# Performance work log

Hardware: AMD Instinct MI355X
Metric: run time of the kernel (lower is better)

## Reference

```python
import jax, jax.numpy as jnp
import numpy as np

# Model dims (see init_kwargs)
E = 512        # embedding_dim
H = 1536       # hidden_dim
SIZE = 4       # state_space.size (state types per layer)
S = 32         # choices per state type (uniform state size)
L = 12         # num_layers of child network
T = SIZE * L   # total controller steps = 48
V = SIZE * S   # num_embeddings = 128


def setup_inputs() -> dict:
    key = jax.random.key(0)
    ks = jax.random.split(key, 12)
    sc = 0.05
    f32 = jnp.float32
    return {
        "input_id": 0,
        "emb":   (jax.random.normal(ks[0], (V, E)) * sc).astype(f32),
        "W_ih1": (jax.random.normal(ks[1], (4 * H, E)) * sc).astype(f32),
        "W_hh1": (jax.random.normal(ks[2], (4 * H, H)) * sc).astype(f32),
        "b_ih1": (jax.random.normal(ks[3], (4 * H,)) * sc).astype(f32),
        "b_hh1": (jax.random.normal(ks[4], (4 * H,)) * sc).astype(f32),
        "W_ih2": (jax.random.normal(ks[5], (4 * H, H)) * sc).astype(f32),
        "W_hh2": (jax.random.normal(ks[6], (4 * H, H)) * sc).astype(f32),
        "b_ih2": (jax.random.normal(ks[7], (4 * H,)) * sc).astype(f32),
        "b_hh2": (jax.random.normal(ks[8], (4 * H,)) * sc).astype(f32),
        "W_out": (jax.random.normal(ks[9], (T, S, H)) * sc).astype(f32),
        "b_out": (jax.random.normal(ks[10], (T, S)) * sc).astype(f32),
    }


def _lstm_cell(x, h, c, Wih, Whh, bih, bhh):
    # torch.nn.LSTMCell: gates ordered (i, f, g, o)
    g = x @ Wih.T + bih + h @ Whh.T + bhh
    gi, gf, gg, go = jnp.split(g, 4)
    c_new = jax.nn.sigmoid(gf) * c + jax.nn.sigmoid(gi) * jnp.tanh(gg)
    h_new = jax.nn.sigmoid(go) * jnp.tanh(c_new)
    return h_new, c_new


def reference(input_id, emb, W_ih1, W_hh1, b_ih1, b_hh1,
              W_ih2, W_hh2, b_ih2, b_hh2, W_out, b_out):
    x0 = emb[input_id]                      # [E]
    z = jnp.zeros((H,), emb.dtype)

    def step(carry, inp):
        i, Wo, bo = inp                     # Wo: [S,H], bo: [S]
        x, h1, c1, h2, c2 = carry
        h1, c1 = _lstm_cell(x, h1, c1, W_ih1, W_hh1, b_ih1, b_hh1)
        h2, c2 = _lstm_cell(h1, h2, c2, W_ih2, W_hh2, b_ih2, b_hh2)
        logp = jax.nn.log_softmax(Wo @ h2 + bo)   # [S]
        pred = jnp.argmax(logp)
        emb_id = (i % SIZE) * S + pred            # state-space embedding id
        x_next = emb[emb_id]
        return (x_next, h1, c1, h2, c2), logp

    _, scores = jax.lax.scan(step, (x0, z, z, z, z),
                             (jnp.arange(T), W_out, b_out))
    return scores  # [T, S] log-probabilities
```

## Files before the change

### kernel.cpp

```cpp
#include <hip/hip_runtime.h>
#include <math.h>

#define H 1536
#define E 512
#define T 48
#define S 32
#define V 128
#define NB 256
#define BT 512
#define JPB 6
#define ROWS 24
#define RPW 3
#define CHK 24
#define WHH2_B   (64 * 145 * 16)
#define HBUF_B   (64 * 7 * 16)
#define DYN_LDS  (WHH2_B + HBUF_B)

#define LOG_W   4096
#define H2_W    20480
#define CAND_W  24576
#define XW1_W   122880

__device__ __forceinline__ float sigf(float x) { return 1.0f / (1.0f + expf(-x)); }
__device__ __forceinline__ float wred(float acc) {
#pragma unroll
    for (int off = 32; off; off >>= 1) acc += __shfl_down(acc, off);
    return acc;
}

#define GLD(p)    __hip_atomic_load((p), __ATOMIC_RELAXED, __HIP_MEMORY_SCOPE_AGENT)
#define GST(p, v) __hip_atomic_store((p), (v), __ATOMIC_RELAXED, __HIP_MEMORY_SCOPE_AGENT)

__device__ __forceinline__ void gbar(unsigned* ctr, unsigned& gen) {
    __syncthreads();
    gen++;
    if (threadIdx.x == 0)
        __hip_atomic_fetch_add(&ctr[(blockIdx.x & 7) * 16], 1u,
                               __ATOMIC_RELAXED, __HIP_MEMORY_SCOPE_AGENT);
    if (threadIdx.x < 8) {
        const unsigned tgt = gen * 32u;
        while (GLD(&ctr[threadIdx.x * 16]) < tgt)
            __builtin_amdgcn_s_sleep(1);
    }
    __syncthreads();
}

__global__ __launch_bounds__(BT, 1) void nas_persist(
    const int* __restrict__ input_id, const float* __restrict__ emb,
    const float* __restrict__ Wih1, const float* __restrict__ Whh1,
    const float* __restrict__ bih1, const float* __restrict__ bhh1,
    const float* __restrict__ Wih2, const float* __restrict__ Whh2,
    const float* __restrict__ bih2, const float* __restrict__ bhh2,
    const float* __restrict__ Wout, const float* __restrict__ bout,
    float* __restrict__ out, float* __restrict__ ws)
{
    const int b = blockIdx.x, tid = threadIdx.x;
    const int wave = tid >> 6, lane = tid & 63;

    unsigned* ctr = (unsigned*)ws;
    float* logitp = ws + LOG_W;
    float* h2gp[2]  = { ws + H2_W,   ws + H2_W + H };
    float* candp[2] = { ws + CAND_W, ws + CAND_W + S * H };
    float* xw1g = ws + XW1_W + (size_t)b * (V * ROWS);

    extern __shared__ char dyn_lds[];
    float4* whh2s = (float4*)dyn_lds;
    float*  hbuf  = (float*)(dyn_lds + WHH2_B);

    __shared__ float gacc1[ROWS], g2f[ROWS], bsum2[ROWS], zlog[S], h2f[JPB];
    __shared__ float c1s[JPB], c2s[JPB], c1cand[S * JPB];
    __shared__ int   xid_s, pred_s;

    unsigned gen = 0;

    if (tid < JPB) { c2s[tid] = 0.f; GST(h2gp[0] + b * JPB + tid, 0.f); }
    if (tid < ROWS) {
        int r = (tid / JPB) * H + b * JPB + (tid % JPB);
        bsum2[tid] = bih2[r] + bhh2[r];
    }
    if (tid == 0) xid_s = *input_id;

    {
        const int k0 = wave * RPW;
        float4 wiA[RPW], wiB[RPW];
        float  bs[RPW];
#pragma unroll
        for (int i = 0; i < RPW; ++i) {
            int k = k0 + i;
            int r = (k / JPB) * H + b * JPB + (k % JPB);
            const float4* w = (const float4*)(Wih1 + (size_t)r * E);
            wiA[i] = w[lane]; wiB[i] = w[lane + 64];
            bs[i]  = bih1[r] + bhh1[r];
        }
        float4* stage = (float4*)dyn_lds;
        for (int ch = 0; ch < 8; ++ch) {
            const float4* src = (const float4*)(emb + (size_t)ch * 16 * E);
            for (int m = tid; m < 2048; m += BT) stage[m] = src[m];
            __syncthreads();
            for (int vv = 0; vv < 16; ++vv) {
                float4 ea = stage[vv * 128 + lane];
                float4 eb = stage[vv * 128 + 64 + lane];
#pragma unroll
                for (int i = 0; i < RPW; ++i) {
                    float a = wiA[i].x * ea.x + wiA[i].y * ea.y + wiA[i].z * ea.z + wiA[i].w * ea.w
                            + wiB[i].x * eb.x + wiB[i].y * eb.y + wiB[i].z * eb.z + wiB[i].w * eb.w;
                    a = wred(a);
                    if (lane == 0) xw1g[(ch * 16 + vv) * ROWS + (k0 + i)] = a + bs[i];
                }
            }
            __syncthreads();
        }
    }

    for (int k = 0; k < ROWS; ++k) {
        int r = (k / JPB) * H + b * JPB + (k % JPB);
        const float4* src = (const float4*)(Whh2 + (size_t)r * H);
        if (tid < 384) {
            int l = tid / 6, j = tid % 6;
            whh2s[l * 145 + k * 6 + j] = src[tid];
        }
    }
    __syncthreads();

    float w1[RPW][CHK], w2[RPW][CHK];
#pragma unroll
    for (int i = 0; i < RPW; ++i) {
        int k = wave * RPW + i;
        int r = (k / JPB) * H + b * JPB + (k % JPB);
        const float4* p1 = (const float4*)(Whh1 + (size_t)r * H) + lane * 6;
        const float4* p2 = (const float4*)(Wih2 + (size_t)r * H) + lane * 6;
#pragma unroll
        for (int j = 0; j < 6; ++j) {
            float4 v1 = p1[j], v2 = p2[j];
            w1[i][4 * j + 0] = v1.x; w1[i][4 * j + 1] = v1.y;
            w1[i][4 * j + 2] = v1.z; w1[i][4 * j + 3] = v1.w;
            w2[i][4 * j + 0] = v2.x; w2[i][4 * j + 1] = v2.y;
            w2[i][4 * j + 2] = v2.z; w2[i][4 * j + 3] = v2.w;
        }
    }
    __syncthreads();

    if (tid < JPB) {
        const float* xr = xw1g + (size_t)xid_s * ROWS;
        float gi = xr[tid], gg = xr[2 * JPB + tid], go = xr[3 * JPB + tid];
        float cn = sigf(gi) * tanhf(gg);
        c1s[tid] = cn;
        GST(candp[0] + b * JPB + tid, sigf(go) * tanhf(cn));
    }
    gbar(ctr, gen);

    const int m0 = (tid / CHK) * 28 + (tid % CHK);
    const int m1 = ((tid + 512) / CHK) * 28 + ((tid + 512) % CHK);
    const int m2 = ((tid + 1024) / CHK) * 28 + ((tid + 1024) % CHK);

    for (int k = 0; k <= T; ++k) {
        float pv[16];
        const float* lp = logitp + (size_t)(k & 1) * (S * NB)
                          + (tid >> 4) * NB + (tid & 15) * 16;
        if (k > 0) {
#pragma unroll
            for (int i = 0; i < 16; ++i) pv[i] = GLD(lp + i);
        }
        const float* h2src = h2gp[k & 1];
        float u0 = GLD(h2src + tid);
        float u1 = GLD(h2src + tid + 512);
        float u2 = GLD(h2src + tid + 1024);
        float wcol[JPB];
        if (k < T && wave == 0 && lane < S) {
            const float* wp = Wout + ((size_t)k * S + lane) * H + b * JPB;
#pragma unroll
            for (int j = 0; j < JPB; ++j) wcol[j] = wp[j];
        }

        if (k > 0) {
            float acc = 0.f;
#pragma unroll
            for (int i = 0; i < 16; ++i) acc += pv[i];
#pragma unroll
            for (int off = 8; off; off >>= 1) acc += __shfl_down(acc, off, 16);
            if ((tid & 15) == 0)
                zlog[tid >> 4] = acc + bout[(size_t)(k - 1) * S + (tid >> 4)];
        }
        __syncthreads();
        if (k > 0) {
            if (wave == 0) {
                float z = (lane < S) ? zlog[lane] : -1e30f;
                float v = z; int idx = (lane < S) ? lane : 9999;
#pragma unroll
                for (int off = 32; off; off >>= 1) {
                    float ov = __shfl_xor(v, off); int oi = __shfl_xor(idx, off);
                    if (ov > v || (ov == v && oi < idx)) { v = ov; idx = oi; }
                }
                float e = (lane < S) ? expf(z - v) : 0.f;
#pragma unroll
                for (int off = 32; off; off >>= 1) e += __shfl_xor(e, off);
                if (lane == 0) pred_s = idx;
                if (b == 0 && lane < S) out[(size_t)(k - 1) * S + lane] = z - v - logf(e);
            }
            __syncthreads();
        }
        if (k == T) return;
        const int psel = (k > 0) ? pred_s : 0;
        if (k > 0 && tid < JPB) c1s[tid] = c1cand[psel * JPB + tid];

        const float* h1src = candp[k & 1] + (size_t)psel * H;
        float t0 = GLD(h1src + tid);
        float t1 = GLD(h1src + tid + 512);
        float t2 = GLD(h1src + tid + 1024);

        hbuf[m0] = u0; hbuf[m1] = u1; hbuf[m2] = u2;
        __syncthreads();
        float h2c[CHK];
        {
            const float4* hp = (const float4*)hbuf + lane * 7;
#pragma unroll
            for (int j = 0; j < 6; ++j) {
                float4 v = hp[j];
                h2c[4 * j + 0] = v.x; h2c[4 * j + 1] = v.y;
                h2c[4 * j + 2] = v.z; h2c[4 * j + 3] = v.w;
            }
        }
        float ahv[RPW];
#pragma unroll
        for (int i = 0; i < RPW; ++i) {
            int kk = wave * RPW + i;
            const float4* wp = whh2s + lane * 145 + kk * 6;
            float ah = 0.f;
#pragma unroll
            for (int j = 0; j < 6; ++j) {
                float4 v = wp[j];
                ah += v.x * h2c[4 * j + 0] + v.y * h2c[4 * j + 1]
                    + v.z * h2c[4 * j + 2] + v.w * h2c[4 * j + 3];
            }
            ahv[i] = wred(ah);
        }
        __syncthreads();
        hbuf[m0] = t0; hbuf[m1] = t1; hbuf[m2] = t2;
        __syncthreads();
        float h1c[CHK];
        {
            const float4* hp = (const float4*)hbuf + lane * 7;
#pragma unroll
            for (int j = 0; j < 6; ++j) {
                float4 v = hp[j];
                h1c[4 * j + 0] = v.x; h1c[4 * j + 1] = v.y;
                h1c[4 * j + 2] = v.z; h1c[4 * j + 3] = v.w;
            }
        }
        float a1[RPW], a2[RPW];
#pragma unroll
        for (int i = 0; i < RPW; ++i) { a1[i] = 0.f; a2[i] = 0.f; }
#pragma unroll
        for (int kk = 0; kk < CHK; ++kk) {
            float h = h1c[kk];
#pragma unroll
            for (int i = 0; i < RPW; ++i) {
                a1[i] += w1[i][kk] * h;
                a2[i] += w2[i][kk] * h;
            }
        }
#pragma unroll
        for (int i = 0; i < RPW; ++i) {
            int kk = wave * RPW + i;
            float s1 = wred(a1[i]);
            float s2 = wred(a2[i]);
            if (lane == 0) {
                gacc1[kk] = s1;
                g2f[kk]   = s2 + ahv[i] + bsum2[kk];
            }
        }
        __syncthreads();

        if (tid < JPB) {
            float gi = g2f[tid],           gf = g2f[JPB + tid];
            float gg = g2f[2 * JPB + tid], go = g2f[3 * JPB + tid];
            float cn = sigf(gf) * c2s[tid] + sigf(gi) * tanhf(gg);
            c2s[tid] = cn;
            float hn = sigf(go) * tanhf(cn);
            h2f[tid] = hn;
            GST(h2gp[(k + 1) & 1] + b * JPB + tid, hn);
        }
        if (tid < S * JPB) {
            int p = tid / JPB, j = tid % JPB;
            const float* xr = xw1g + (size_t)((k & 3) * S + p) * ROWS;
            float gi = gacc1[j]           + xr[j];
            float gf = gacc1[JPB + j]     + xr[JPB + j];
            float gg = gacc1[2 * JPB + j] + xr[2 * JPB + j];
            float go = gacc1[3 * JPB + j] + xr[3 * JPB + j];
            float cn = sigf(gf) * c1s[j] + sigf(gi) * tanhf(gg);
            c1cand[tid] = cn;
            GST(candp[(k + 1) & 1] + (size_t)p * H + b * JPB + j,
                sigf(go) * tanhf(cn));
        }
        __syncthreads();
        if (wave == 0 && lane < S) {
            float p = 0.f;
#pragma unroll
            for (int j = 0; j < JPB; ++j) p += wcol[j] * h2f[j];
            GST(logitp + (size_t)((k + 1) & 1) * (S * NB) + lane * NB + b, p);
        }
        gbar(ctr, gen);
    }
}

extern "C" void kernel_launch(void* const* d_in, const int* in_sizes, int n_in,
                              void* d_out, int out_size, void* d_ws, size_t ws_size,
                              hipStream_t stream) {
    const int*   input_id = (const int*)d_in[0];
    const float* emb  = (const float*)d_in[1];
    const float* Wih1 = (const float*)d_in[2];
    const float* Whh1 = (const float*)d_in[3];
    const float* bih1 = (const float*)d_in[4];
    const float* bhh1 = (const float*)d_in[5];
    const float* Wih2 = (const float*)d_in[6];
    const float* Whh2 = (const float*)d_in[7];
    const float* bih2 = (const float*)d_in[8];
    const float* bhh2 = (const float*)d_in[9];
    const float* Wout = (const float*)d_in[10];
    const float* bout = (const float*)d_in[11];
    float* out = (float*)d_out;
    float* ws  = (float*)d_ws;

    hipMemsetAsync(d_ws, 0, 512, stream);

    void* args[] = { (void*)&input_id, (void*)&emb,
                     (void*)&Wih1, (void*)&Whh1, (void*)&bih1, (void*)&bhh1,
                     (void*)&Wih2, (void*)&Whh2, (void*)&bih2, (void*)&bhh2,
                     (void*)&Wout, (void*)&bout, (void*)&out, (void*)&ws };
    hipLaunchCooperativeKernel((void*)nas_persist, dim3(NB), dim3(BT), args,
                               DYN_LDS, stream);
}
```

Measured before the change: 1.207 ms.

## Replace atomic grid barrier with generation-tagged logit partials as dataflow flags

```diff
diff --git a/kernel.cpp b/kernel.cpp
--- a/kernel.cpp
+++ b/kernel.cpp
@@ -16,10 +16,11 @@
 #define HBUF_B   (64 * 7 * 16)
 #define DYN_LDS  (WHH2_B + HBUF_B)
 
-#define LOG_W   4096
-#define H2_W    20480
-#define CAND_W  24576
-#define XW1_W   122880
+typedef unsigned long long u64;
+
+#define H2_W    32768
+#define CAND_W  36864
+#define XW1_W   135168
 
 __device__ __forceinline__ float sigf(float x) { return 1.0f / (1.0f + expf(-x)); }
 __device__ __forceinline__ float wred(float acc) {
@@ -28,24 +29,18 @@
     return acc;
 }
 
-#define GLD(p)    __hip_atomic_load((p), __ATOMIC_RELAXED, __HIP_MEMORY_SCOPE_AGENT)
-#define GST(p, v) __hip_atomic_store((p), (v), __ATOMIC_RELAXED, __HIP_MEMORY_SCOPE_AGENT)
-
-__device__ __forceinline__ void gbar(unsigned* ctr, unsigned& gen) {
-    __syncthreads();
-    gen++;
-    if (threadIdx.x == 0)
-        __hip_atomic_fetch_add(&ctr[(blockIdx.x & 7) * 16], 1u,
-                               __ATOMIC_RELAXED, __HIP_MEMORY_SCOPE_AGENT);
-    if (threadIdx.x < 8) {
-        const unsigned tgt = gen * 32u;
-        while (GLD(&ctr[threadIdx.x * 16]) < tgt)
-            __builtin_amdgcn_s_sleep(1);
-    }
-    __syncthreads();
+#define GLD(p)      __hip_atomic_load((p), __ATOMIC_RELAXED, __HIP_MEMORY_SCOPE_AGENT)
+#define GST(p, v)   __hip_atomic_store((p), (v), __ATOMIC_RELAXED, __HIP_MEMORY_SCOPE_AGENT)
+#define GLD64(p)    __hip_atomic_load((p), __ATOMIC_RELAXED, __HIP_MEMORY_SCOPE_AGENT)
+#define GST64(p, v) __hip_atomic_store((p), (v), __ATOMIC_RELAXED, __HIP_MEMORY_SCOPE_AGENT)
+
+__device__ __forceinline__ u64 pkf(float v, unsigned g) {
+    return ((u64)g << 32) | (u64)__float_as_uint(v);
 }
-
-__global__ __launch_bounds__(BT, 1) void nas_persist(
+__device__ __forceinline__ float    pvf(u64 x) { return __uint_as_float((unsigned)x); }
+__device__ __forceinline__ unsigned ptg(u64 x) { return (unsigned)(x >> 32); }
+
+__global__ __launch_bounds__(BT, 2) void nas_persist(
     const int* __restrict__ input_id, const float* __restrict__ emb,
     const float* __restrict__ Wih1, const float* __restrict__ Whh1,
     const float* __restrict__ bih1, const float* __restrict__ bhh1,
@@ -57,8 +52,7 @@
     const int b = blockIdx.x, tid = threadIdx.x;
     const int wave = tid >> 6, lane = tid & 63;
 
-    unsigned* ctr = (unsigned*)ws;
-    float* logitp = ws + LOG_W;
+    u64* logitt = (u64*)ws;
     float* h2gp[2]  = { ws + H2_W,   ws + H2_W + H };
     float* candp[2] = { ws + CAND_W, ws + CAND_W + S * H };
     float* xw1g = ws + XW1_W + (size_t)b * (V * ROWS);
@@ -70,8 +64,6 @@
     __shared__ float gacc1[ROWS], g2f[ROWS], bsum2[ROWS], zlog[S], h2f[JPB];
     __shared__ float c1s[JPB], c2s[JPB], c1cand[S * JPB];
     __shared__ int   xid_s, pred_s;
-
-    unsigned gen = 0;
 
     if (tid < JPB) { c2s[tid] = 0.f; GST(h2gp[0] + b * JPB + tid, 0.f); }
     if (tid < ROWS) {
@@ -147,35 +139,51 @@
         c1s[tid] = cn;
         GST(candp[0] + b * JPB + tid, sigf(go) * tanhf(cn));
     }
-    gbar(ctr, gen);
+    __syncthreads();
+    if (wave == 0 && lane < S)
+        GST64(logitt + lane * NB + b, pkf(0.f, 1u));
 
     const int m0 = (tid / CHK) * 28 + (tid % CHK);
     const int m1 = ((tid + 512) / CHK) * 28 + ((tid + 512) % CHK);
     const int m2 = ((tid + 1024) / CHK) * 28 + ((tid + 1024) % CHK);
 
     for (int k = 0; k <= T; ++k) {
-        float pv[16];
-        const float* lp = logitp + (size_t)(k & 1) * (S * NB)
-                          + (tid >> 4) * NB + (tid & 15) * 16;
-        if (k > 0) {
-#pragma unroll
-            for (int i = 0; i < 16; ++i) pv[i] = GLD(lp + i);
-        }
+        const unsigned expg = (unsigned)(k + 1);
+
+        u64 pv[16];
+        const u64* lp = logitt + (size_t)(k & 1) * (S * NB)
+                        + (tid >> 4) * NB + (tid & 15) * 16;
+#pragma unroll
+        for (int i = 0; i < 16; ++i) pv[i] = GLD64(lp + i);
+
+        float wcol[JPB];
+        if (k < T && wave == 0 && lane < S) {
+            const float* wp = Wout + ((size_t)k * S + lane) * H + b * JPB;
+#pragma unroll
+            for (int j = 0; j < JPB; ++j) wcol[j] = wp[j];
+        }
+
+        for (;;) {
+            bool ok = true;
+#pragma unroll
+            for (int i = 0; i < 16; ++i) ok &= (ptg(pv[i]) >= expg);
+            if (ok) break;
+            __builtin_amdgcn_s_sleep(1);
+#pragma unroll
+            for (int i = 0; i < 16; ++i)
+                if (ptg(pv[i]) < expg) pv[i] = GLD64(lp + i);
+        }
+        __syncthreads();
+
         const float* h2src = h2gp[k & 1];
         float u0 = GLD(h2src + tid);
         float u1 = GLD(h2src + tid + 512);
         float u2 = GLD(h2src + tid + 1024);
-        float wcol[JPB];
-        if (k < T && wave == 0 && lane < S) {
-            const float* wp = Wout + ((size_t)k * S + lane) * H + b * JPB;
-#pragma unroll
-            for (int j = 0; j < JPB; ++j) wcol[j] = wp[j];
-        }
 
         if (k > 0) {
             float acc = 0.f;
 #pragma unroll
-            for (int i = 0; i < 16; ++i) acc += pv[i];
+            for (int i = 0; i < 16; ++i) acc += pvf(pv[i]);
 #pragma unroll
             for (int off = 8; off; off >>= 1) acc += __shfl_down(acc, off, 16);
             if ((tid & 15) == 0)
@@ -297,9 +305,9 @@
             float p = 0.f;
 #pragma unroll
             for (int j = 0; j < JPB; ++j) p += wcol[j] * h2f[j];
-            GST(logitp + (size_t)((k + 1) & 1) * (S * NB) + lane * NB + b, p);
-        }
-        gbar(ctr, gen);
+            GST64(logitt + (size_t)((k + 1) & 1) * (S * NB) + lane * NB + b,
+                  pkf(p, (unsigned)(k + 2)));
+        }
     }
 }
 
@@ -321,7 +329,7 @@
     float* out = (float*)d_out;
     float* ws  = (float*)d_ws;
 
-    hipMemsetAsync(d_ws, 0, 512, stream);
+    hipMemsetAsync(d_ws, 0, 2 * S * NB * sizeof(u64), stream);
 
     void* args[] = { (void*)&input_id, (void*)&emb,
                      (void*)&Wih1, (void*)&Whh1, (void*)&bih1, (void*)&bhh1,
```

Result: slower. 1.767 ms (+46.4%).
